# Optimization experiments

Measured on AMD Instinct MI355X. Metric: run time of the kernel, lower is better.

Reference implementation:

```python
import jax, jax.numpy as jnp
import numpy as np


def conv1x1(x, w, b):
    # 1x1 conv: x [B,C,H,W], w [O,C], b [O]
    return jnp.einsum('bchw,oc->bohw', x, w) + b[None, :, None, None]


def _propagate(x, w_red, b_red, w_u, b_u, w_lam, b_lam, w_wt, b_wt, direction):
    transposed = direction in ('lr', 'rl')
    reverse = direction in ('bt', 'rl')
    prop_dim = 2 if direction in ('tb', 'bt') else 3
    reduced = conv1x1(x, w_red, b_red)
    u = conv1x1(reduced, w_u, b_u)
    lam = conv1x1(reduced, w_lam, b_lam)
    pre = conv1x1(reduced, w_wt, b_wt)
    if transposed:
        x, lam, pre, u = (t.swapaxes(-1, -2) for t in (x, lam, pre, u))
    if reverse:
        x, lam, pre, u = (jnp.flip(t, axis=prop_dim) for t in (x, lam, pre, u))
    S = x.shape[prop_dim]  # square input: H == W == S
    # sigmoid + channel-normalize the 3 tridiagonal band weights
    wn = jax.nn.sigmoid(pre)
    wn = wn / jnp.maximum(wn.sum(axis=1, keepdims=True), 1e-6)
    # In the original, hidden is broadcast identically over the row's j entries,
    # so (hidden[...,None]*tridiag_row).sum(-1) == hidden * rowsum(tridiag_row).
    # Row i has band entries at j = i-1, i, i+1 (where in range), all valued wn[:,k,...,i].
    wk = wn if prop_dim == 2 else wn.swapaxes(2, 3)  # [B,3,m,i]
    idx = jnp.arange(S)
    valid = jnp.stack([idx >= 1, jnp.ones((S,), bool), idx <= S - 2]).astype(wk.dtype)  # [3,S]
    R = (wk * valid[None, :, None, :]).sum(axis=1)  # [B,m,i] tridiagonal row-sums
    Rseq = jnp.moveaxis(R, -1, 0)  # [S,B,m]
    step_axis = 2 if transposed else 3  # axis of x indexed per step (as in original)
    Xseq = jnp.moveaxis(x, step_axis, 0)       # [S,B,C,m]
    Lseq = jnp.moveaxis(lam, 5 - step_axis, 0)  # lambda indexed on the other spatial axis

    def step(h, inp):
        r, xi, li = inp
        h = h * r[:, None, :] + li * xi
        return h, h

    h0 = jnp.zeros_like(Xseq[0])  # [B,C,m]
    _, ys = jax.lax.scan(step, h0, (Rseq, Xseq, Lseq))  # ys [S,B,C,m]
    out = jnp.moveaxis(ys, 0, 2 if transposed else 3)
    if reverse:
        out = jnp.flip(out, axis=prop_dim)
    out = out * u
    if transposed:
        out = out.swapaxes(-1, -2)
    return out


def _forward(x, w_red, b_red, w_u, b_u, w_lam, b_lam, w_wt, b_wt, w_merge, b_merge):
    outs = [_propagate(x, w_red, b_red, w_u, b_u, w_lam, b_lam, w_wt, b_wt, d)
            for d in ('tb', 'bt', 'lr', 'rl')]
    concat = jnp.concatenate(outs, axis=1)  # [B,4C,H,W]
    # NOTE: the original also computes a softmax-merged tensor that is discarded;
    # the returned output is merge(concat) only.
    return conv1x1(concat, w_merge, b_merge)


def setup_inputs() -> dict:
    key = jax.random.key(0)
    ks = jax.random.split(key, 11)
    B, C, S = 8, 256, 64
    Cr = C // 4
    f32 = jnp.float32
    x = jax.random.normal(ks[0], (B, C, S, S), f32)
    w_red = jax.random.normal(ks[1], (Cr, C), f32) * C ** -0.5
    b_red = jax.random.normal(ks[2], (Cr,), f32) * 0.01
    w_u = jax.random.normal(ks[3], (C, Cr), f32) * Cr ** -0.5
    b_u = jax.random.normal(ks[4], (C,), f32) * 0.01
    w_lam = jax.random.normal(ks[5], (C, Cr), f32) * Cr ** -0.5
    b_lam = jax.random.normal(ks[6], (C,), f32) * 0.01
    w_wt = jax.random.normal(ks[7], (3, Cr), f32) * Cr ** -0.5
    b_wt = jax.random.normal(ks[8], (3,), f32) * 0.01
    w_merge = jax.random.normal(ks[9], (C, 4 * C), f32) * (4 * C) ** -0.5
    b_merge = jax.random.normal(ks[10], (C,), f32) * 0.01
    return {"x": x, "w_red": w_red, "b_red": b_red, "w_u": w_u, "b_u": b_u,
            "w_lam": w_lam, "b_lam": b_lam, "w_wt": w_wt, "b_wt": b_wt,
            "w_merge": w_merge, "b_merge": b_merge}


def reference(x, w_red, b_red, w_u, b_u, w_lam, b_lam, w_wt, b_wt, w_merge, b_merge):
    return _forward(x, w_red, b_red, w_u, b_u, w_lam, b_lam, w_wt, b_wt, w_merge, b_merge)
```

## Files before the change

kernel.cpp:

```cpp
#include <hip/hip_runtime.h>


typedef __attribute__((ext_vector_type(8))) short short8b;
typedef __attribute__((ext_vector_type(4))) float f32x4;
typedef __attribute__((ext_vector_type(2))) unsigned int uint2v;
typedef __attribute__((ext_vector_type(4))) unsigned int uint4v;

__device__ __forceinline__ unsigned short bf16_rne(float v) {
  unsigned u = __float_as_uint(v);
  unsigned r = u + 0x7FFF + ((u >> 16) & 1);
  return (unsigned short)(r >> 16);
}
__device__ __forceinline__ float bf16_f(unsigned short h) {
  return __uint_as_float((unsigned)h << 16);
}

#define TR_READ8(q0,q1,q2,q3,q4,q5,q6,q7,va0,va1,va2,va3)                      \
  asm volatile("ds_read_b64_tr_b16 %0, %8\n\t"                                 \
               "ds_read_b64_tr_b16 %1, %8 offset:128\n\t"                      \
               "ds_read_b64_tr_b16 %2, %9\n\t"                                 \
               "ds_read_b64_tr_b16 %3, %9 offset:128\n\t"                      \
               "ds_read_b64_tr_b16 %4, %10\n\t"                                \
               "ds_read_b64_tr_b16 %5, %10 offset:128\n\t"                     \
               "ds_read_b64_tr_b16 %6, %11\n\t"                                \
               "ds_read_b64_tr_b16 %7, %11 offset:128\n\t"                     \
               "s_waitcnt lgkmcnt(0)"                                          \
               : "=&v"(q0), "=&v"(q1), "=&v"(q2), "=&v"(q3),                   \
                 "=&v"(q4), "=&v"(q5), "=&v"(q6), "=&v"(q7)                    \
               : "v"(va0), "v"(va1), "v"(va2), "v"(va3))

__global__ __launch_bounds__(256) void k_prep(const float* __restrict__ w_red,
    const float* __restrict__ w_merge, const float* __restrict__ w_u,
    const float* __restrict__ w_lam, float* __restrict__ wredT,
    unsigned short* __restrict__ wu2, unsigned short* __restrict__ wlam2,
    unsigned short* __restrict__ W2T) {
  int idx = blockIdx.x * 256 + threadIdx.x;
  if (idx < 16384) { int c = idx >> 6, k = idx & 63; wredT[idx] = w_red[k * 256 + c]; }
  int j = idx - 16384;
  if (j >= 0 && j < 16384) wu2[j] = bf16_rne(w_u[j]);
  int l = idx - 32768;
  if (l >= 0 && l < 16384) wlam2[l] = bf16_rne(w_lam[l]);
  int m = idx - 49152;
  if (m >= 0 && m < 131072) {
    int o = m >> 9, cc = m & 511;
    float v = w_merge[o * 1024 + cc] + w_merge[o * 1024 + cc + 512];
    W2T[m] = bf16_rne(v);
  }
}

__global__ __launch_bounds__(256) void k_red(const float* __restrict__ x,
    const float* __restrict__ wredT, const float* __restrict__ b_red,
    const float* __restrict__ w_wt, const float* __restrict__ b_wt,
    unsigned short* __restrict__ red2, float* __restrict__ R0) {
  __shared__ float xs[64][68];
  __shared__ float ws[64][68];
  int b = blockIdx.y;
  int px0 = blockIdx.x * 64;
  int t = threadIdx.x;
  int pxg = t & 15, mg = t >> 4;
  float acc[4][4] = {};
  for (int ch = 0; ch < 4; ch++) {
    int c0 = ch * 64;
#pragma unroll
    for (int i = 0; i < 4; i++) {
      int idx4 = i * 256 + t;
      int kk = idx4 >> 4, j4 = idx4 & 15;
      *(float4*)&xs[kk][j4 * 4] =
          *(const float4*)(x + ((size_t)b << 20) + ((size_t)(c0 + kk) << 12) + px0 + j4 * 4);
      *(float4*)&ws[kk][j4 * 4] = *(const float4*)(wredT + ((c0 + kk) << 6) + j4 * 4);
    }
    __syncthreads();
#pragma unroll 8
    for (int kk = 0; kk < 64; kk++) {
      float4 a = *(float4*)&xs[kk][pxg * 4];
      float4 w = *(float4*)&ws[kk][mg * 4];
      float aa[4] = {a.x, a.y, a.z, a.w}, wv[4] = {w.x, w.y, w.z, w.w};
#pragma unroll
      for (int j = 0; j < 4; j++)
#pragma unroll
        for (int i = 0; i < 4; i++) acc[j][i] = fmaf(wv[j], aa[i], acc[j][i]);
    }
    __syncthreads();
  }
#pragma unroll
  for (int j = 0; j < 4; j++) {
    int m = mg * 4 + j;
    float bv = b_red[m];
    float v0 = acc[j][0] + bv, v1 = acc[j][1] + bv, v2 = acc[j][2] + bv, v3 = acc[j][3] + bv;
    ushort4 uv = make_ushort4(bf16_rne(v0), bf16_rne(v1), bf16_rne(v2), bf16_rne(v3));
    *(ushort4*)(red2 + ((size_t)b << 18) + ((size_t)m << 12) + px0 + pxg * 4) = uv;
    float* d = &xs[m][pxg * 4];
    d[0] = v0; d[1] = v1; d[2] = v2; d[3] = v3;
  }
  __syncthreads();
  float* preS = &ws[0][0];
  if (t < 192) {
    int j = t >> 6, px = t & 63;
    float a = b_wt[j];
    for (int kk = 0; kk < 64; kk++) a = fmaf(w_wt[j * 64 + kk], xs[kk][px], a);
    preS[j * 64 + px] = a;
  }
  __syncthreads();
  if (t < 64) {
    float s0 = 1.f / (1.f + __expf(-preS[t]));
    float s1 = 1.f / (1.f + __expf(-preS[64 + t]));
    float s2 = 1.f / (1.f + __expf(-preS[128 + t]));
    int w = t;
    float num = s1 + (w >= 1 ? s0 : 0.f) + (w <= 62 ? s2 : 0.f);
    R0[((size_t)b << 12) + px0 + t] = num / fmaxf(s0 + s1 + s2, 1e-6f);
  }
}

__global__ __launch_bounds__(256) void k_ulam(const unsigned short* __restrict__ red2,
    const unsigned short* __restrict__ wu2, const float* __restrict__ b_u,
    const unsigned short* __restrict__ wlam2, const float* __restrict__ b_lam,
    unsigned short* __restrict__ u, unsigned short* __restrict__ lam) {
  __shared__ __align__(16) unsigned short WL[256 * 72];
  __shared__ __align__(16) unsigned short PL[4096];
  const int t = threadIdx.x;
  const int px0 = blockIdx.x * 64;
  const int b = blockIdx.y;
  const int mt = blockIdx.z;
  const unsigned short* Wsrc = (mt == 0) ? wu2 : wlam2;
  const float* bias = (mt == 0) ? b_u : b_lam;
  unsigned short* dst = (mt == 0) ? u : lam;
  const unsigned short* red2b = red2 + ((size_t)b << 18);
  const int lane = t & 63;
  const int ln15 = lane & 15, lg = lane >> 4;
  const int ow = (t >> 6) * 64;

#pragma unroll
  for (int i = 0; i < 8; i++) {
    int unit = i * 256 + t, wrow = unit >> 3, wp = unit & 7;
    *(short8b*)&WL[wrow * 72 + wp * 8] = *(const short8b*)(Wsrc + wrow * 64 + wp * 8);
  }
#pragma unroll
  for (int i = 0; i < 2; i++) {
    int unit = i * 256 + t, kk = unit >> 3, ap = unit & 7;
    int off = ((ap >> 1) << 10) + ((kk >> 2) << 6) + ((kk & 3) << 4) + (ap & 1) * 8;
    *(short8b*)&PL[off] = *(const short8b*)(red2b + (size_t)kk * 4096 + px0 + ap * 8);
  }
  __syncthreads();

  f32x4 acc[4][4];
#pragma unroll
  for (int i = 0; i < 4; i++)
#pragma unroll
    for (int j = 0; j < 4; j++) acc[i][j] = (f32x4){0.f, 0.f, 0.f, 0.f};

  const unsigned pbase = (unsigned)(size_t)(&PL[0]);
  const unsigned vab = pbase + (unsigned)(lg * 256 + ln15 * 8);
#pragma unroll
  for (int kstep = 0; kstep < 2; kstep++) {
    short8b am[4];
#pragma unroll
    for (int i = 0; i < 4; i++)
      am[i] = *(const short8b*)&WL[(ow + i * 16 + ln15) * 72 + kstep * 32 + lg * 8];
    unsigned va0 = vab + kstep * 1024;
    unsigned va1 = va0 + 2048, va2 = va0 + 4096, va3 = va0 + 6144;
    uint2v q0, q1, q2, q3, q4, q5, q6, q7;
    TR_READ8(q0, q1, q2, q3, q4, q5, q6, q7, va0, va1, va2, va3);
    __builtin_amdgcn_sched_barrier(0);
    uint4v bu[4] = {(uint4v){q0.x, q0.y, q1.x, q1.y}, (uint4v){q2.x, q2.y, q3.x, q3.y},
                    (uint4v){q4.x, q4.y, q5.x, q5.y}, (uint4v){q6.x, q6.y, q7.x, q7.y}};
#pragma unroll
    for (int i = 0; i < 4; i++)
#pragma unroll
      for (int j = 0; j < 4; j++)
        acc[i][j] = __builtin_amdgcn_mfma_f32_16x16x32_bf16(
            am[i], __builtin_bit_cast(short8b, bu[j]), acc[i][j], 0, 0, 0);
  }

#pragma unroll
  for (int i = 0; i < 4; i++) {
    int orow = ow + i * 16 + lg * 4;
    float bm[4];
#pragma unroll
    for (int r = 0; r < 4; r++) bm[r] = bias[orow + r];
#pragma unroll
    for (int j = 0; j < 4; j++) {
      int pxc = px0 + j * 16 + ln15;
#pragma unroll
      for (int r = 0; r < 4; r++)
        dst[((size_t)b << 20) + ((size_t)(orow + r) << 12) + pxc] =
            bf16_rne(acc[i][j][r] + bm[r]);
    }
  }
}

__global__ __launch_bounds__(256) void k_scan(const float* __restrict__ x,
    const unsigned short* __restrict__ lam, const unsigned short* __restrict__ u,
    const float* __restrict__ R0, unsigned short* __restrict__ P2,
    unsigned short* __restrict__ Q2) {
  __shared__ __align__(16) char smem[20224];
  float* lamS = (float*)smem;
  unsigned* outS = (unsigned*)smem;
  float* fixS = (float*)(smem + 16896);
  const int t = threadIdx.x;
  const int c = blockIdx.x;
  const int b = blockIdx.y;
  const size_t ibase = ((size_t)b << 20) + ((size_t)c << 12);

  {
    const unsigned short* lp = lam + ibase;
#pragma unroll
    for (int i = 0; i < 2; i++) {
      int unit = i * 256 + t;
      int row = unit >> 3, c8 = unit & 7;
      short8b v = *(const short8b*)(lp + row * 64 + c8 * 8);
      float* d = &lamS[row * 65 + c8 * 8];
#pragma unroll
      for (int j = 0; j < 8; j++) d[j] = bf16_f((unsigned short)v[j]);
    }
  }
  const int r = t & 63;
  const int qc = __builtin_amdgcn_readfirstlane(t >> 6);
  float xr[16], R[16];
  {
    const float* xp = x + ibase + (r << 6) + (qc << 4);
    const float* rp = R0 + ((size_t)b << 12) + (r << 6) + (qc << 4);
#pragma unroll
    for (int i = 0; i < 4; i++) {
      float4 v = *(const float4*)(xp + i * 4);
      xr[i * 4] = v.x; xr[i * 4 + 1] = v.y; xr[i * 4 + 2] = v.z; xr[i * 4 + 3] = v.w;
      float4 w = *(const float4*)(rp + i * 4);
      R[i * 4] = w.x; R[i * 4 + 1] = w.y; R[i * 4 + 2] = w.z; R[i * 4 + 3] = w.w;
    }
  }
  __syncthreads();
  float g1[16], g2[16];
  float A = 1.f, B1 = 0.f, B2 = 0.f;
#pragma unroll
  for (int j = 0; j < 16; j++) {
    int w = (qc << 4) + j;
    float l1 = lamS[w * 65 + r];
    float l2 = lamS[(63 - w) * 65 + (63 - r)];
    g1[j] = l1 * xr[j];
    g2[j] = l2 * xr[j];
    A *= R[j];
    B1 = fmaf(B1, R[j], g1[j]);
    B2 = fmaf(B2, R[j], g2[j]);
  }
  __syncthreads();
  fixS[r * 13 + qc * 3 + 0] = A;
  fixS[r * 13 + qc * 3 + 1] = B1;
  fixS[r * 13 + qc * 3 + 2] = B2;
  __syncthreads();
  float h1 = 0.f, h2 = 0.f;
  for (int p = 0; p < qc; p++) {
    float Ap  = fixS[r * 13 + p * 3 + 0];
    float Bp1 = fixS[r * 13 + p * 3 + 1];
    float Bp2 = fixS[r * 13 + p * 3 + 2];
    h1 = fmaf(h1, Ap, Bp1);
    h2 = fmaf(h2, Ap, Bp2);
  }
  float ur[16], fr[16];
  {
    const unsigned short* up = u + ibase + (r << 6) + (qc << 4);
    const unsigned short* fp = u + ibase + ((size_t)(63 - r) << 6) + (qc << 4);
    short8b u0 = *(const short8b*)(up);
    short8b u1 = *(const short8b*)(up + 8);
    short8b f0 = *(const short8b*)(fp);
    short8b f1 = *(const short8b*)(fp + 8);
#pragma unroll
    for (int j = 0; j < 8; j++) {
      ur[j] = bf16_f((unsigned short)u0[j]); ur[8 + j] = bf16_f((unsigned short)u1[j]);
      fr[j] = bf16_f((unsigned short)f0[j]); fr[8 + j] = bf16_f((unsigned short)f1[j]);
    }
  }
#pragma unroll
  for (int j2 = 0; j2 < 8; j2++) {
    int j = j2 * 2;
    h1 = fmaf(h1, R[j], g1[j]);         float p0 = h1 * ur[j];
    h2 = fmaf(h2, R[j], g2[j]);         float q0 = h2 * fr[j];
    h1 = fmaf(h1, R[j + 1], g1[j + 1]); float p1 = h1 * ur[j + 1];
    h2 = fmaf(h2, R[j + 1], g2[j + 1]); float q1 = h2 * fr[j + 1];
    int ob = r * 33 + (qc << 3) + j2;
    outS[ob]        = (unsigned)bf16_rne(p0) | ((unsigned)bf16_rne(p1) << 16);
    outS[2112 + ob] = (unsigned)bf16_rne(q0) | ((unsigned)bf16_rne(q1) << 16);
  }
  __syncthreads();
#pragma unroll
  for (int i = 0; i < 4; i++) {
    int flat4 = i * 256 + t;
    int s = flat4 >> 9;
    int rem = flat4 & 511;
    int row = rem >> 3, c8 = rem & 7;
    const unsigned* ls = &outS[s * 2112 + row * 33 + c8 * 4];
    uint4 v = make_uint4(ls[0], ls[1], ls[2], ls[3]);
    unsigned short* base = (s == 0) ? P2 : Q2;
    size_t off = ((size_t)(b * 256 + c)) * 4096 + row * 64 + c8 * 8;
    *(uint4*)(base + off) = v;
  }
}

__global__ __launch_bounds__(256) void k_merge(
    const unsigned short* __restrict__ P2, const unsigned short* __restrict__ Q2,
    const unsigned short* __restrict__ W2T, const float* __restrict__ b_merge,
    float* __restrict__ out) {
  __shared__ __align__(16) unsigned short WL[256 * 72];
  __shared__ __align__(16) unsigned short PL[4096];
  const int t = threadIdx.x;
  const int px0 = blockIdx.x * 64;
  const int b = blockIdx.y;
  const int lane = t & 63;
  const int ln15 = lane & 15, lg = lane >> 4;
  const int ow = (t >> 6) * 64;

  const unsigned short* P2b = P2 + (size_t)b * 256 * 4096;
  const unsigned short* Q2b = Q2 + (size_t)b * 256 * 4096;

  f32x4 acc[4][4];
#pragma unroll
  for (int i = 0; i < 4; i++)
#pragma unroll
    for (int j = 0; j < 4; j++) acc[i][j] = (f32x4){0.f, 0.f, 0.f, 0.f};

  short8b wreg[8], preg[2];
#pragma unroll
  for (int i = 0; i < 8; i++) {
    int unit = i * 256 + t, wrow = unit >> 3, wp = unit & 7;
    wreg[i] = *(const short8b*)(W2T + (size_t)wrow * 512 + wp * 8);
  }
#pragma unroll
  for (int i = 0; i < 2; i++) {
    int unit = i * 256 + t, kk = unit >> 3, ap = unit & 7;
    preg[i] = *(const short8b*)(P2b + (size_t)kk * 4096 + px0 + ap * 8);
  }

  const unsigned pbase = (unsigned)(size_t)(&PL[0]);
  const unsigned vab = pbase + (unsigned)(lg * 256 + ln15 * 8);

  for (int it = 0; it < 8; ++it) {
    __syncthreads();
#pragma unroll
    for (int i = 0; i < 8; i++) {
      int unit = i * 256 + t, wrow = unit >> 3, wp = unit & 7;
      *(short8b*)&WL[wrow * 72 + wp * 8] = wreg[i];
    }
#pragma unroll
    for (int i = 0; i < 2; i++) {
      int unit = i * 256 + t, kk = unit >> 3, ap = unit & 7;
      int off = ((ap >> 1) << 10) + ((kk >> 2) << 6) + ((kk & 3) << 4) + (ap & 1) * 8;
      *(short8b*)&PL[off] = preg[i];
    }
    __syncthreads();
    if (it < 7) {
      int nt = it + 1;
#pragma unroll
      for (int i = 0; i < 8; i++) {
        int unit = i * 256 + t, wrow = unit >> 3, wp = unit & 7;
        wreg[i] = *(const short8b*)(W2T + (size_t)wrow * 512 + nt * 64 + wp * 8);
      }
      const unsigned short* ps = (nt < 4) ? P2b : Q2b;
      int row0 = (nt & 3) * 64;
#pragma unroll
      for (int i = 0; i < 2; i++) {
        int unit = i * 256 + t, kk = unit >> 3, ap = unit & 7;
        preg[i] = *(const short8b*)(ps + (size_t)(row0 + kk) * 4096 + px0 + ap * 8);
      }
    }
#pragma unroll
    for (int kstep = 0; kstep < 2; kstep++) {
      short8b am[4];
#pragma unroll
      for (int i = 0; i < 4; i++)
        am[i] = *(const short8b*)&WL[(ow + i * 16 + ln15) * 72 + kstep * 32 + lg * 8];
      unsigned va0 = vab + kstep * 1024;
      unsigned va1 = va0 + 2048, va2 = va0 + 4096, va3 = va0 + 6144;
      uint2v q0, q1, q2, q3, q4, q5, q6, q7;
      TR_READ8(q0, q1, q2, q3, q4, q5, q6, q7, va0, va1, va2, va3);
      __builtin_amdgcn_sched_barrier(0);
      uint4v bu[4] = {(uint4v){q0.x, q0.y, q1.x, q1.y}, (uint4v){q2.x, q2.y, q3.x, q3.y},
                      (uint4v){q4.x, q4.y, q5.x, q5.y}, (uint4v){q6.x, q6.y, q7.x, q7.y}};
#pragma unroll
      for (int i = 0; i < 4; i++)
#pragma unroll
        for (int j = 0; j < 4; j++)
          acc[i][j] = __builtin_amdgcn_mfma_f32_16x16x32_bf16(
              am[i], __builtin_bit_cast(short8b, bu[j]), acc[i][j], 0, 0, 0);
    }
  }

#pragma unroll
  for (int i = 0; i < 4; i++) {
    int orow = ow + i * 16 + lg * 4;
    float bm[4];
#pragma unroll
    for (int r = 0; r < 4; r++) bm[r] = b_merge[orow + r];
#pragma unroll
    for (int j = 0; j < 4; j++) {
      int pxc = px0 + j * 16 + ln15;
      float* op = out + ((size_t)b << 20) + ((size_t)orow << 12) + pxc;
#pragma unroll
      for (int r = 0; r < 4; r++) op[(size_t)r << 12] = acc[i][j][r] + bm[r];
    }
  }
}

extern "C" void kernel_launch(void* const* d_in, const int* in_sizes, int n_in,
                              void* d_out, int out_size, void* d_ws, size_t ws_size,
                              hipStream_t stream) {
  const float* x       = (const float*)d_in[0];
  const float* w_red   = (const float*)d_in[1];
  const float* b_red   = (const float*)d_in[2];
  const float* w_u     = (const float*)d_in[3];
  const float* b_u     = (const float*)d_in[4];
  const float* w_lam   = (const float*)d_in[5];
  const float* b_lam   = (const float*)d_in[6];
  const float* w_wt    = (const float*)d_in[7];
  const float* b_wt    = (const float*)d_in[8];
  const float* w_merge = (const float*)d_in[9];
  const float* b_merge = (const float*)d_in[10];
  float* out = (float*)d_out;
  char* wsb = (char*)d_ws;

  float* wredT          = (float*)(wsb);
  unsigned short* wu2   = (unsigned short*)(wsb + 65536);
  unsigned short* wlam2 = (unsigned short*)(wsb + 98304);
  unsigned short* red2  = (unsigned short*)(wsb + 131072);
  unsigned short* u     = (unsigned short*)(wsb + 4325376);
  unsigned short* lam   = (unsigned short*)(wsb + 21102592);
  float* R0             = (float*)(wsb + 37879808);
  unsigned short* W2T   = (unsigned short*)(wsb + 38010880);
  unsigned short* P2    = (unsigned short*)(wsb + 38273024);
  unsigned short* Q2    = (unsigned short*)(wsb + 55050240);

  hipLaunchKernelGGL(k_prep,  dim3(704),      dim3(256), 0, stream,
                     w_red, w_merge, w_u, w_lam, wredT, wu2, wlam2, W2T);
  hipLaunchKernelGGL(k_red,   dim3(64, 8),    dim3(256), 0, stream, x, wredT, b_red,
                     w_wt, b_wt, red2, R0);
  hipLaunchKernelGGL(k_ulam,  dim3(64, 8, 2), dim3(256), 0, stream, red2, wu2, b_u,
                     wlam2, b_lam, u, lam);
  hipLaunchKernelGGL(k_scan,  dim3(256, 8),   dim3(256), 0, stream, x, lam, u, R0, P2, Q2);
  hipLaunchKernelGGL(k_merge, dim3(64, 8),    dim3(256), 0, stream, P2, Q2, W2T, b_merge, out);
}
```

Measured before the change: 77.63 us.

## Fuse weight prep, channel reduction and u/lambda projections into one front kernel

Merges k_prep, k_red and k_ulam into a single k_front kernel. The reduced activations stay in shared memory as bf16 in the transposed MFMA layout and are never written to or re-read from global memory. Weight transposition and bf16 conversion for w_red, w_u and w_lam now happen inline inside each block, and two extra block columns handle the w_merge preprocessing. This removes two kernel launches and the red2 global round trip. In exchange each block does redundant weight conversion, runs eight sequential MFMA chunks with syncs, and launches only 528 blocks instead of 1024 for the projection work.

```diff
diff --git a/kernel.cpp b/kernel.cpp
--- a/kernel.cpp
+++ b/kernel.cpp
@@ -29,35 +29,35 @@
                  "=&v"(q4), "=&v"(q5), "=&v"(q6), "=&v"(q7)                    \
                : "v"(va0), "v"(va1), "v"(va2), "v"(va3))
 
-__global__ __launch_bounds__(256) void k_prep(const float* __restrict__ w_red,
-    const float* __restrict__ w_merge, const float* __restrict__ w_u,
-    const float* __restrict__ w_lam, float* __restrict__ wredT,
-    unsigned short* __restrict__ wu2, unsigned short* __restrict__ wlam2,
-    unsigned short* __restrict__ W2T) {
-  int idx = blockIdx.x * 256 + threadIdx.x;
-  if (idx < 16384) { int c = idx >> 6, k = idx & 63; wredT[idx] = w_red[k * 256 + c]; }
-  int j = idx - 16384;
-  if (j >= 0 && j < 16384) wu2[j] = bf16_rne(w_u[j]);
-  int l = idx - 32768;
-  if (l >= 0 && l < 16384) wlam2[l] = bf16_rne(w_lam[l]);
-  int m = idx - 49152;
-  if (m >= 0 && m < 131072) {
-    int o = m >> 9, cc = m & 511;
-    float v = w_merge[o * 1024 + cc] + w_merge[o * 1024 + cc + 512];
-    W2T[m] = bf16_rne(v);
-  }
-}
-
-__global__ __launch_bounds__(256) void k_red(const float* __restrict__ x,
-    const float* __restrict__ wredT, const float* __restrict__ b_red,
+__global__ __launch_bounds__(256) void k_front(const float* __restrict__ x,
+    const float* __restrict__ w_red, const float* __restrict__ b_red,
     const float* __restrict__ w_wt, const float* __restrict__ b_wt,
-    unsigned short* __restrict__ red2, float* __restrict__ R0) {
+    const float* __restrict__ w_u, const float* __restrict__ b_u,
+    const float* __restrict__ w_lam, const float* __restrict__ b_lam,
+    const float* __restrict__ w_merge,
+    unsigned short* __restrict__ u, unsigned short* __restrict__ lam,
+    float* __restrict__ R0, unsigned short* __restrict__ W2T) {
+  const int t = threadIdx.x;
+  if (blockIdx.x >= 64) {
+    int e = (blockIdx.x - 64) * 8 + blockIdx.y;
+#pragma unroll
+    for (int i = 0; i < 32; i++) {
+      int m = e * 8192 + i * 256 + t;
+      int o = m >> 9, cc = m & 511;
+      float v = w_merge[o * 1024 + cc] + w_merge[o * 1024 + cc + 512];
+      W2T[m] = bf16_rne(v);
+    }
+    return;
+  }
   __shared__ float xs[64][68];
   __shared__ float ws[64][68];
-  int b = blockIdx.y;
-  int px0 = blockIdx.x * 64;
-  int t = threadIdx.x;
-  int pxg = t & 15, mg = t >> 4;
+  unsigned short* WL = (unsigned short*)&xs[0][0];
+  float* preS = &ws[0][0];
+  unsigned short* PL = (unsigned short*)((char*)&ws[0][0] + 4096);
+  const int b = blockIdx.y;
+  const int px0 = blockIdx.x * 64;
+  const int pxg = t & 15, mg = t >> 4;
+
   float acc[4][4] = {};
   for (int ch = 0; ch < 4; ch++) {
     int c0 = ch * 64;
@@ -67,7 +67,18 @@
       int kk = idx4 >> 4, j4 = idx4 & 15;
       *(float4*)&xs[kk][j4 * 4] =
           *(const float4*)(x + ((size_t)b << 20) + ((size_t)(c0 + kk) << 12) + px0 + j4 * 4);
-      *(float4*)&ws[kk][j4 * 4] = *(const float4*)(wredT + ((c0 + kk) << 6) + j4 * 4);
+    }
+    {
+      int row = t >> 2, q = t & 3;
+      const float* wp = w_red + row * 256 + c0 + q * 16;
+      float4 va = *(const float4*)(wp);
+      float4 vb = *(const float4*)(wp + 4);
+      float4 vc = *(const float4*)(wp + 8);
+      float4 vd = *(const float4*)(wp + 12);
+      float tmp[16] = {va.x, va.y, va.z, va.w, vb.x, vb.y, vb.z, vb.w,
+                       vc.x, vc.y, vc.z, vc.w, vd.x, vd.y, vd.z, vd.w};
+#pragma unroll
+      for (int jj = 0; jj < 16; jj++) ws[q * 16 + jj][row] = tmp[jj];
     }
     __syncthreads();
 #pragma unroll 8
@@ -84,16 +95,21 @@
   }
 #pragma unroll
   for (int j = 0; j < 4; j++) {
-    int m = mg * 4 + j;
-    float bv = b_red[m];
-    float v0 = acc[j][0] + bv, v1 = acc[j][1] + bv, v2 = acc[j][2] + bv, v3 = acc[j][3] + bv;
-    ushort4 uv = make_ushort4(bf16_rne(v0), bf16_rne(v1), bf16_rne(v2), bf16_rne(v3));
-    *(ushort4*)(red2 + ((size_t)b << 18) + ((size_t)m << 12) + px0 + pxg * 4) = uv;
-    float* d = &xs[m][pxg * 4];
-    d[0] = v0; d[1] = v1; d[2] = v2; d[3] = v3;
-  }
-  __syncthreads();
-  float* preS = &ws[0][0];
+    int k = mg * 4 + j;
+    float bv = b_red[k];
+    float v[4];
+#pragma unroll
+    for (int i = 0; i < 4; i++) v[i] = acc[j][i] + bv;
+    float* d = &xs[k][pxg * 4];
+    d[0] = v[0]; d[1] = v[1]; d[2] = v[2]; d[3] = v[3];
+#pragma unroll
+    for (int i = 0; i < 4; i++) {
+      int pxl = pxg * 4 + i;
+      int off = ((pxl >> 4) << 10) + ((k >> 2) << 6) + ((k & 3) << 4) + (pxl & 15);
+      PL[off] = bf16_rne(v[i]);
+    }
+  }
+  __syncthreads();
   if (t < 192) {
     int j = t >> 6, px = t & 63;
     float a = b_wt[j];
@@ -109,81 +125,60 @@
     float num = s1 + (w >= 1 ? s0 : 0.f) + (w <= 62 ? s2 : 0.f);
     R0[((size_t)b << 12) + px0 + t] = num / fmaxf(s0 + s1 + s2, 1e-6f);
   }
-}
-
-__global__ __launch_bounds__(256) void k_ulam(const unsigned short* __restrict__ red2,
-    const unsigned short* __restrict__ wu2, const float* __restrict__ b_u,
-    const unsigned short* __restrict__ wlam2, const float* __restrict__ b_lam,
-    unsigned short* __restrict__ u, unsigned short* __restrict__ lam) {
-  __shared__ __align__(16) unsigned short WL[256 * 72];
-  __shared__ __align__(16) unsigned short PL[4096];
-  const int t = threadIdx.x;
-  const int px0 = blockIdx.x * 64;
-  const int b = blockIdx.y;
-  const int mt = blockIdx.z;
-  const unsigned short* Wsrc = (mt == 0) ? wu2 : wlam2;
-  const float* bias = (mt == 0) ? b_u : b_lam;
-  unsigned short* dst = (mt == 0) ? u : lam;
-  const unsigned short* red2b = red2 + ((size_t)b << 18);
   const int lane = t & 63;
   const int ln15 = lane & 15, lg = lane >> 4;
-  const int ow = (t >> 6) * 64;
-
-#pragma unroll
-  for (int i = 0; i < 8; i++) {
-    int unit = i * 256 + t, wrow = unit >> 3, wp = unit & 7;
-    *(short8b*)&WL[wrow * 72 + wp * 8] = *(const short8b*)(Wsrc + wrow * 64 + wp * 8);
-  }
-#pragma unroll
-  for (int i = 0; i < 2; i++) {
-    int unit = i * 256 + t, kk = unit >> 3, ap = unit & 7;
-    int off = ((ap >> 1) << 10) + ((kk >> 2) << 6) + ((kk & 3) << 4) + (ap & 1) * 8;
-    *(short8b*)&PL[off] = *(const short8b*)(red2b + (size_t)kk * 4096 + px0 + ap * 8);
-  }
-  __syncthreads();
-
-  f32x4 acc[4][4];
-#pragma unroll
-  for (int i = 0; i < 4; i++)
-#pragma unroll
-    for (int j = 0; j < 4; j++) acc[i][j] = (f32x4){0.f, 0.f, 0.f, 0.f};
-
-  const unsigned pbase = (unsigned)(size_t)(&PL[0]);
+  const int wv = t >> 6;
+  const unsigned pbase = (unsigned)(size_t)PL;
   const unsigned vab = pbase + (unsigned)(lg * 256 + ln15 * 8);
-#pragma unroll
-  for (int kstep = 0; kstep < 2; kstep++) {
-    short8b am[4];
-#pragma unroll
-    for (int i = 0; i < 4; i++)
-      am[i] = *(const short8b*)&WL[(ow + i * 16 + ln15) * 72 + kstep * 32 + lg * 8];
-    unsigned va0 = vab + kstep * 1024;
-    unsigned va1 = va0 + 2048, va2 = va0 + 4096, va3 = va0 + 6144;
-    uint2v q0, q1, q2, q3, q4, q5, q6, q7;
-    TR_READ8(q0, q1, q2, q3, q4, q5, q6, q7, va0, va1, va2, va3);
-    __builtin_amdgcn_sched_barrier(0);
-    uint4v bu[4] = {(uint4v){q0.x, q0.y, q1.x, q1.y}, (uint4v){q2.x, q2.y, q3.x, q3.y},
-                    (uint4v){q4.x, q4.y, q5.x, q5.y}, (uint4v){q6.x, q6.y, q7.x, q7.y}};
-#pragma unroll
-    for (int i = 0; i < 4; i++)
+  for (int mc = 0; mc < 8; ++mc) {
+    const float* Wsrc = (mc < 4) ? w_u : w_lam;
+    const float* bias = (mc < 4) ? b_u : b_lam;
+    unsigned short* dst = (mc < 4) ? u : lam;
+    int m0 = (mc & 3) * 64;
+    __syncthreads();
+    {
+      int row = t >> 2, q = t & 3;
+      const float* wp = Wsrc + (m0 + row) * 64 + q * 16;
+      float4 va = *(const float4*)(wp);
+      float4 vb = *(const float4*)(wp + 4);
+      float4 vc = *(const float4*)(wp + 8);
+      float4 vd = *(const float4*)(wp + 12);
+      float tmp[16] = {va.x, va.y, va.z, va.w, vb.x, vb.y, vb.z, vb.w,
+                       vc.x, vc.y, vc.z, vc.w, vd.x, vd.y, vd.z, vd.w};
+      unsigned short* dw = &WL[row * 72 + q * 16];
+#pragma unroll
+      for (int jj = 0; jj < 16; jj++) dw[jj] = bf16_rne(tmp[jj]);
+    }
+    __syncthreads();
+    f32x4 ac[4];
+#pragma unroll
+    for (int j = 0; j < 4; j++) ac[j] = (f32x4){0.f, 0.f, 0.f, 0.f};
+#pragma unroll
+    for (int kstep = 0; kstep < 2; kstep++) {
+      short8b am = *(const short8b*)&WL[(wv * 16 + ln15) * 72 + kstep * 32 + lg * 8];
+      unsigned va0 = vab + kstep * 1024;
+      unsigned va1 = va0 + 2048, va2 = va0 + 4096, va3 = va0 + 6144;
+      uint2v q0, q1, q2, q3, q4, q5, q6, q7;
+      TR_READ8(q0, q1, q2, q3, q4, q5, q6, q7, va0, va1, va2, va3);
+      __builtin_amdgcn_sched_barrier(0);
+      uint4v bu[4] = {(uint4v){q0.x, q0.y, q1.x, q1.y}, (uint4v){q2.x, q2.y, q3.x, q3.y},
+                      (uint4v){q4.x, q4.y, q5.x, q5.y}, (uint4v){q6.x, q6.y, q7.x, q7.y}};
 #pragma unroll
       for (int j = 0; j < 4; j++)
-        acc[i][j] = __builtin_amdgcn_mfma_f32_16x16x32_bf16(
-            am[i], __builtin_bit_cast(short8b, bu[j]), acc[i][j], 0, 0, 0);
-  }
-
-#pragma unroll
-  for (int i = 0; i < 4; i++) {
-    int orow = ow + i * 16 + lg * 4;
+        ac[j] = __builtin_amdgcn_mfma_f32_16x16x32_bf16(
+            am, __builtin_bit_cast(short8b, bu[j]), ac[j], 0, 0, 0);
+    }
+    int orow = wv * 16 + lg * 4;
     float bm[4];
 #pragma unroll
-    for (int r = 0; r < 4; r++) bm[r] = bias[orow + r];
+    for (int r = 0; r < 4; r++) bm[r] = bias[m0 + orow + r];
 #pragma unroll
     for (int j = 0; j < 4; j++) {
       int pxc = px0 + j * 16 + ln15;
 #pragma unroll
       for (int r = 0; r < 4; r++)
-        dst[((size_t)b << 20) + ((size_t)(orow + r) << 12) + pxc] =
-            bf16_rne(acc[i][j][r] + bm[r]);
+        dst[((size_t)b << 20) + ((size_t)(m0 + orow + r) << 12) + pxc] =
+            bf16_rne(ac[j][r] + bm[r]);
     }
   }
 }
@@ -415,23 +410,16 @@
   float* out = (float*)d_out;
   char* wsb = (char*)d_ws;
 
-  float* wredT          = (float*)(wsb);
-  unsigned short* wu2   = (unsigned short*)(wsb + 65536);
-  unsigned short* wlam2 = (unsigned short*)(wsb + 98304);
-  unsigned short* red2  = (unsigned short*)(wsb + 131072);
-  unsigned short* u     = (unsigned short*)(wsb + 4325376);
-  unsigned short* lam   = (unsigned short*)(wsb + 21102592);
-  float* R0             = (float*)(wsb + 37879808);
-  unsigned short* W2T   = (unsigned short*)(wsb + 38010880);
-  unsigned short* P2    = (unsigned short*)(wsb + 38273024);
-  unsigned short* Q2    = (unsigned short*)(wsb + 55050240);
-
-  hipLaunchKernelGGL(k_prep,  dim3(704),      dim3(256), 0, stream,
-                     w_red, w_merge, w_u, w_lam, wredT, wu2, wlam2, W2T);
-  hipLaunchKernelGGL(k_red,   dim3(64, 8),    dim3(256), 0, stream, x, wredT, b_red,
-                     w_wt, b_wt, red2, R0);
-  hipLaunchKernelGGL(k_ulam,  dim3(64, 8, 2), dim3(256), 0, stream, red2, wu2, b_u,
-                     wlam2, b_lam, u, lam);
-  hipLaunchKernelGGL(k_scan,  dim3(256, 8),   dim3(256), 0, stream, x, lam, u, R0, P2, Q2);
-  hipLaunchKernelGGL(k_merge, dim3(64, 8),    dim3(256), 0, stream, P2, Q2, W2T, b_merge, out);
-}
+  unsigned short* u   = (unsigned short*)(wsb);
+  unsigned short* lam = (unsigned short*)(wsb + 16777216);
+  float* R0           = (float*)(wsb + 33554432);
+  unsigned short* W2T = (unsigned short*)(wsb + 33685504);
+  unsigned short* P2  = (unsigned short*)(wsb + 33947648);
+  unsigned short* Q2  = (unsigned short*)(wsb + 50724864);
+
+  hipLaunchKernelGGL(k_front, dim3(66, 8),  dim3(256), 0, stream,
+                     x, w_red, b_red, w_wt, b_wt, w_u, b_u, w_lam, b_lam, w_merge,
+                     u, lam, R0, W2T);
+  hipLaunchKernelGGL(k_scan,  dim3(256, 8), dim3(256), 0, stream, x, lam, u, R0, P2, Q2);
+  hipLaunchKernelGGL(k_merge, dim3(64, 8),  dim3(256), 0, stream, P2, Q2, W2T, b_merge, out);
+}
```

After: 79.79 us. 1.03x slower.
